# Kernel optimization log

Measured on AMD Instinct MI355X. Metric: run time of the kernel, lower is better.

Reference implementation:

```python
import jax, jax.numpy as jnp
import numpy as np

TEMPERATURE = 0.07
EPS = 1e-12  # F.normalize clamp


def _project(x, We, be, W1, b1, W2, b2):
    # encoder Linear then projection head Linear->ReLU->Linear
    h = x @ We + be                      # [B, 512]
    h = jax.nn.relu(h @ W1 + b1)         # [B, 256]
    return h @ W2 + b2                   # [B, 128]


def _ntxent(z1, z2, t):
    B = z1.shape[0]
    z1 = z1 / jnp.maximum(jnp.linalg.norm(z1, axis=1, keepdims=True), EPS)
    z2 = z2 / jnp.maximum(jnp.linalg.norm(z2, axis=1, keepdims=True), EPS)
    reps = jnp.concatenate([z1, z2], axis=0)          # [2B, 128]
    sim = reps @ reps.T                               # [2B, 2B]
    N = 2 * B
    idx = jnp.arange(N)
    # positives: eye rolled by B along columns -> column (i+B) mod N
    pos = sim[idx, (idx + B) % N][:, None]            # [N, 1]
    # negatives: all off-diagonal entries per row, in column order
    cols = jnp.arange(N - 1)[None, :]                 # [1, N-1]
    neg_idx = cols + (cols >= idx[:, None])           # skip the diagonal
    neg = jnp.take_along_axis(sim, neg_idx, axis=1)   # [N, N-1]
    logits = jnp.concatenate([pos, neg], axis=1) / t  # [N, N]
    # cross-entropy with label 0
    return jnp.mean(jax.nn.logsumexp(logits, axis=1) - logits[:, 0])


def setup_inputs() -> dict:
    key = jax.random.key(0)
    ks = jax.random.split(key, 10)
    B, Din, Denc, Dh, Dp = 4096, 1024, 512, 256, 128
    s = lambda fan_in: 1.0 / np.sqrt(fan_in)
    return {
        "x_image": jax.random.normal(ks[0], (B, Din), jnp.float32),
        "x_text": jax.random.normal(ks[1], (B, Din), jnp.float32),
        "We_img": jax.random.normal(ks[2], (Din, Denc), jnp.float32) * s(Din),
        "be_img": jnp.zeros((Denc,), jnp.float32),
        "We_txt": jax.random.normal(ks[3], (Din, Denc), jnp.float32) * s(Din),
        "be_txt": jnp.zeros((Denc,), jnp.float32),
        "Wp1_img": jax.random.normal(ks[4], (Denc, Dh), jnp.float32) * s(Denc),
        "bp1_img": jnp.zeros((Dh,), jnp.float32),
        "Wp2_img": jax.random.normal(ks[5], (Dh, Dp), jnp.float32) * s(Dh),
        "bp2_img": jnp.zeros((Dp,), jnp.float32),
        "Wp1_txt": jax.random.normal(ks[6], (Denc, Dh), jnp.float32) * s(Denc),
        "bp1_txt": jnp.zeros((Dh,), jnp.float32),
        "Wp2_txt": jax.random.normal(ks[7], (Dh, Dp), jnp.float32) * s(Dh),
        "bp2_txt": jnp.zeros((Dp,), jnp.float32),
    }


def reference(x_image, x_text, We_img, be_img, We_txt, be_txt,
              Wp1_img, bp1_img, Wp2_img, bp2_img,
              Wp1_txt, bp1_txt, Wp2_txt, bp2_txt):
    z1 = _project(x_image, We_img, be_img, Wp1_img, bp1_img, Wp2_img, bp2_img)
    z2 = _project(x_text, We_txt, be_txt, Wp1_txt, bp1_txt, Wp2_txt, bp2_txt)
    # single modality pair ('image','text') -> one NT-Xent loss
    return _ntxent(z1, z2, TEMPERATURE)
```

## Files before the change

### kernel.cpp

```cpp
#include <hip/hip_runtime.h>
#include <hip/hip_bf16.h>
#include <math.h>

typedef __bf16 bf16_t;
typedef __bf16 bf8 __attribute__((ext_vector_type(8)));
typedef __bf16 bf4 __attribute__((ext_vector_type(4)));
typedef __bf16 bf16x2 __attribute__((ext_vector_type(2)));
typedef float f32x4 __attribute__((ext_vector_type(4)));

#define AS1 __attribute__((address_space(1)))
#define AS3 __attribute__((address_space(3)))

#define B_ROWS 4096
#define NTOT   8192
#define DIN    1024
#define DENC   512
#define DH     256
#define DP     128
#define NSLICE 16
#define INV_T        14.285714285714286f
#define SCALE_LOG2   20.609929155556620f

__device__ __forceinline__ f32x4 mfma_16x16x32(bf8 a, bf8 b, f32x4 c) {
  return __builtin_amdgcn_mfma_f32_16x16x32_bf16(a, b, c, 0, 0, 0);
}

__global__ __launch_bounds__(256) void prep_kernel(
    const float* __restrict__ x_i, const float* __restrict__ x_t,
    const float* __restrict__ We_i, const float* __restrict__ We_t,
    const float* __restrict__ W1_i, const float* __restrict__ W1_t,
    const float* __restrict__ W2_i, const float* __restrict__ W2_t,
    bf16_t* __restrict__ xb_i, bf16_t* __restrict__ xb_t,
    bf16_t* __restrict__ Wet_i, bf16_t* __restrict__ Wet_t,
    bf16_t* __restrict__ W1t_i, bf16_t* __restrict__ W1t_t,
    bf16_t* __restrict__ W2t_i, bf16_t* __restrict__ W2t_t) {
  const int b = blockIdx.x;
  const int tid = threadIdx.x;
  if (b >= 336) {
    int idx = (b - 336) * 256 + tid;
    const int HALF = (B_ROWS * DIN) / 4;
    const float* s; bf16_t* d; int off;
    if (idx < HALF) { s = x_i; d = xb_i; off = idx; }
    else            { s = x_t; d = xb_t; off = idx - HALF; }
    float4 v = ((const float4*)s)[off];
    bf4 w = { (bf16_t)v.x, (bf16_t)v.y, (bf16_t)v.z, (bf16_t)v.w };
    ((bf4*)d)[off] = w;
    return;
  }
  const float* src; bf16_t* dst; int K, N, tile;
  if (b < 128)      { src = We_i; dst = Wet_i; K = 1024; N = 512; tile = b; }
  else if (b < 256) { src = We_t; dst = Wet_t; K = 1024; N = 512; tile = b - 128; }
  else if (b < 288) { src = W1_i; dst = W1t_i; K = 512;  N = 256; tile = b - 256; }
  else if (b < 320) { src = W1_t; dst = W1t_t; K = 512;  N = 256; tile = b - 288; }
  else if (b < 328) { src = W2_i; dst = W2t_i; K = 256;  N = 128; tile = b - 320; }
  else              { src = W2_t; dst = W2t_t; K = 256;  N = 128; tile = b - 328; }
  const int tilesN = N >> 6;
  const int k0 = (tile / tilesN) * 64;
  const int n0 = (tile % tilesN) * 64;

  __shared__ float ld[64][65];
  #pragma unroll
  for (int i = 0; i < 4; ++i) {
    int cid = tid + i * 256;
    int r = cid >> 4;
    int c = (cid & 15) * 4;
    float4 v = *(const float4*)(src + (size_t)(k0 + r) * N + n0 + c);
    ld[r][c + 0] = v.x; ld[r][c + 1] = v.y; ld[r][c + 2] = v.z; ld[r][c + 3] = v.w;
  }
  __syncthreads();
  #pragma unroll
  for (int i = 0; i < 2; ++i) {
    int cid = tid + i * 256;
    int rn = cid >> 3;
    int c8 = (cid & 7) * 8;
    bf8 w;
    #pragma unroll
    for (int j = 0; j < 8; ++j) w[j] = (bf16_t)ld[c8 + j][rn];
    *(bf8*)(dst + (size_t)(n0 + rn) * K + k0 + c8) = w;
  }
}

template<int MT, bool RELU>
__global__ __launch_bounds__(256) void gemm_glds(
    const bf16_t* __restrict__ A0, const bf16_t* __restrict__ A1,
    const bf16_t* __restrict__ B0, const bf16_t* __restrict__ B1,
    const float* __restrict__ bias0, const float* __restrict__ bias1,
    bf16_t* __restrict__ out0, bf16_t* __restrict__ out1,
    int N, int K) {
  const bf16_t* A   = blockIdx.z ? A1 : A0;
  const bf16_t* Bt  = blockIdx.z ? B1 : B0;
  const float* bias = blockIdx.z ? bias1 : bias0;
  bf16_t* outp      = blockIdx.z ? out1 : out0;

  const int nb   = blockIdx.x * 64;
  const int mb   = blockIdx.y * MT;
  const int tid  = threadIdx.x;
  const int wave = tid >> 6;
  const int lane = tid & 63;
  const int l15  = lane & 15;
  const int quad = lane >> 4;
  constexpr int CH = MT / 64;

  __shared__ __align__(16) bf16_t As[2][MT * 32];
  __shared__ __align__(16) bf16_t Bs[2][64 * 32];

  f32x4 acc[CH][4];
  #pragma unroll
  for (int i = 0; i < CH; ++i)
    #pragma unroll
    for (int j = 0; j < 4; ++j) acc[i][j] = (f32x4){0.f, 0.f, 0.f, 0.f};

  auto stage = [&](int k0, int pb) {
    #pragma unroll
    for (int i = 0; i < CH; ++i) {
      const int s = tid + i * 256;
      const bf16_t* ga = A + (size_t)(mb + (s >> 2)) * K + k0 + (s & 3) * 8;
      __builtin_amdgcn_global_load_lds(
          (const AS1 void*)ga,
          (AS3 void*)(As[pb] + (size_t)(wave * 64 + i * 256) * 8), 16, 0, 0);
    }
    const bf16_t* gb = Bt + (size_t)(nb + (tid >> 2)) * K + k0 + (tid & 3) * 8;
    __builtin_amdgcn_global_load_lds(
        (const AS1 void*)gb,
        (AS3 void*)(Bs[pb] + (size_t)(wave * 64) * 8), 16, 0, 0);
  };

  stage(0, 0);
  const int T = K >> 5;
  for (int t = 0; t < T; ++t) {
    __syncthreads();
    if (t + 1 < T) stage((t + 1) << 5, (t + 1) & 1);
    const bf16_t* as = As[t & 1];
    const bf16_t* bs = Bs[t & 1];
    bf8 a[CH];
    #pragma unroll
    for (int i = 0; i < CH; ++i)
      a[i] = *(const bf8*)(as + (size_t)(wave * (16 * CH) + i * 16 + l15) * 32 + quad * 8);
    #pragma unroll
    for (int nt = 0; nt < 4; ++nt) {
      bf8 bb = *(const bf8*)(bs + (size_t)(nt * 16 + l15) * 32 + quad * 8);
      #pragma unroll
      for (int i = 0; i < CH; ++i)
        acc[i][nt] = mfma_16x16x32(a[i], bb, acc[i][nt]);
    }
  }

  #pragma unroll
  for (int i = 0; i < CH; ++i) {
    const int orow = mb + wave * (16 * CH) + i * 16 + quad * 4;
    #pragma unroll
    for (int nt = 0; nt < 4; ++nt) {
      const int ocol = nb + nt * 16 + l15;
      const float bval = bias[ocol];
      #pragma unroll
      for (int r = 0; r < 4; ++r) {
        float v = acc[i][nt][r] + bval;
        if (RELU) v = fmaxf(v, 0.f);
        outp[(size_t)(orow + r) * N + ocol] = (bf16_t)v;
      }
    }
  }
}

__global__ __launch_bounds__(256) void head2_norm(
    const bf16_t* __restrict__ A0, const bf16_t* __restrict__ A1,
    const bf16_t* __restrict__ B0, const bf16_t* __restrict__ B1,
    const float* __restrict__ bias0, const float* __restrict__ bias1,
    bf16_t* __restrict__ reps) {
  const bf16_t* A   = blockIdx.z ? A1 : A0;
  const bf16_t* Bt  = blockIdx.z ? B1 : B0;
  const float* bias = blockIdx.z ? bias1 : bias0;

  const int mb   = blockIdx.x * 16;
  const int tid  = threadIdx.x;
  const int wave = tid >> 6;
  const int lane = tid & 63;
  const int l15  = lane & 15;
  const int quad = lane >> 4;
  const int wc0  = wave * 32;

  __shared__ __align__(16) bf16_t Asb[2][16 * 32];
  __shared__ __align__(16) bf16_t Bsb[2][128 * 32];
  __shared__ float ssL[64];

  f32x4 acc[2];
  acc[0] = (f32x4){0.f, 0.f, 0.f, 0.f};
  acc[1] = (f32x4){0.f, 0.f, 0.f, 0.f};

  auto stage = [&](int k0, int pb) {
    if (wave == 0) {
      const int row = lane >> 2, j = lane & 3, cf = j ^ (row & 3);
      const bf16_t* ga = A + (size_t)(mb + row) * DH + k0 + cf * 8;
      __builtin_amdgcn_global_load_lds(
          (const AS1 void*)ga, (AS3 void*)(Asb[pb]), 16, 0, 0);
    }
    #pragma unroll
    for (int i = 0; i < 2; ++i) {
      const int s = wave * 64 + i * 256 + lane;
      const int col = s >> 2, j = s & 3, cf = j ^ (col & 3);
      const bf16_t* gb = Bt + (size_t)col * DH + k0 + cf * 8;
      __builtin_amdgcn_global_load_lds(
          (const AS1 void*)gb,
          (AS3 void*)(Bsb[pb] + (size_t)(wave * 64 + i * 256) * 8), 16, 0, 0);
    }
  };

  stage(0, 0);
  for (int t = 0; t < 8; ++t) {
    __syncthreads();
    if (t < 7) stage((t + 1) << 5, (t + 1) & 1);
    const bf16_t* as = Asb[t & 1];
    const bf16_t* bs = Bsb[t & 1];
    bf8 a = *(const bf8*)(as + (size_t)(l15 * 4 + (quad ^ (l15 & 3))) * 8);
    #pragma unroll
    for (int nt = 0; nt < 2; ++nt) {
      const int col = wc0 + nt * 16 + l15;
      bf8 bb = *(const bf8*)(bs + (size_t)(col * 4 + (quad ^ (col & 3))) * 8);
      acc[nt] = mfma_16x16x32(a, bb, acc[nt]);
    }
  }

  float ssp[4];
  #pragma unroll
  for (int r = 0; r < 4; ++r) {
    #pragma unroll
    for (int nt = 0; nt < 2; ++nt) acc[nt][r] += bias[wc0 + nt * 16 + l15];
    float s = acc[0][r] * acc[0][r] + acc[1][r] * acc[1][r];
    s += __shfl_xor(s, 1); s += __shfl_xor(s, 2);
    s += __shfl_xor(s, 4); s += __shfl_xor(s, 8);
    ssp[r] = s;
  }
  if (l15 == 0) {
    #pragma unroll
    for (int r = 0; r < 4; ++r) ssL[wave * 16 + quad * 4 + r] = ssp[r];
  }
  __syncthreads();
  const size_t gr0 = (size_t)(blockIdx.z ? B_ROWS : 0) + mb + quad * 4;
  #pragma unroll
  for (int r = 0; r < 4; ++r) {
    const int row = quad * 4 + r;
    float tot = ssL[row] + ssL[16 + row] + ssL[32 + row] + ssL[48 + row];
    const float inv = 1.0f / fmaxf(sqrtf(tot), 1e-12f);
    #pragma unroll
    for (int nt = 0; nt < 2; ++nt)
      reps[(gr0 + r) * DP + wc0 + nt * 16 + l15] = (bf16_t)(acc[nt][r] * inv);
  }
}

__global__ __launch_bounds__(256) void sim_rowsum_kernel(
    const bf16_t* __restrict__ reps, float* __restrict__ Spart) {
  const int rowbase = blockIdx.y * 256;
  const int slice   = blockIdx.x;
  const int col0    = slice * 512;
  const int tid  = threadIdx.x;
  const int wave = tid >> 6;
  const int lane = tid & 63;
  const int l15  = lane & 15;
  const int quad = lane >> 4;

  __shared__ __align__(16) bf16_t Bs[2][64 * DP];

  const int r0 = rowbase + wave * 64;
  bf8 af[4][4];
  #pragma unroll
  for (int c = 0; c < 4; ++c)
    #pragma unroll
    for (int kt = 0; kt < 4; ++kt)
      af[c][kt] = *(const bf8*)(reps + (size_t)(r0 + c * 16 + l15) * DP + kt * 32 + quad * 8);

  float rs[4][4];
  #pragma unroll
  for (int c = 0; c < 4; ++c)
    #pragma unroll
    for (int r = 0; r < 4; ++r) rs[c][r] = 0.f;

  for (int t = 0; t < 8; ++t) {
    bf16_t* buf = Bs[t & 1];
    __syncthreads();
    const int jt0 = col0 + t * 64;
    #pragma unroll
    for (int r = 0; r < 4; ++r) {
      const int s   = r * 256 + tid;
      const int col = s >> 4;
      const int cf  = (s & 15) ^ (col & 15);
      const bf16_t* g = reps + (size_t)(jt0 + col) * DP + cf * 8;
      __builtin_amdgcn_global_load_lds(
          (const AS1 void*)g,
          (AS3 void*)(buf + (size_t)(r * 256 + wave * 64) * 8), 16, 0, 0);
    }
    __syncthreads();

    #pragma unroll
    for (int st = 0; st < 4; ++st) {
      const bf16_t* base = buf + (size_t)(st * 16 + l15) * DP;
      bf8 b0 = *(const bf8*)(base + (((0 * 4 + quad) ^ l15) * 8));
      bf8 b1 = *(const bf8*)(base + (((1 * 4 + quad) ^ l15) * 8));
      bf8 b2 = *(const bf8*)(base + (((2 * 4 + quad) ^ l15) * 8));
      bf8 b3 = *(const bf8*)(base + (((3 * 4 + quad) ^ l15) * 8));
      #pragma unroll
      for (int c = 0; c < 4; ++c) {
        f32x4 acc = (f32x4){0.f, 0.f, 0.f, 0.f};
        acc = mfma_16x16x32(af[c][0], b0, acc);
        acc = mfma_16x16x32(af[c][1], b1, acc);
        acc = mfma_16x16x32(af[c][2], b2, acc);
        acc = mfma_16x16x32(af[c][3], b3, acc);
        #pragma unroll
        for (int r = 0; r < 4; ++r)
          rs[c][r] += __builtin_amdgcn_exp2f(acc[r] * SCALE_LOG2);
      }
    }
  }

  #pragma unroll
  for (int c = 0; c < 4; ++c) {
    const int i0 = r0 + c * 16 + quad * 4;
    #pragma unroll
    for (int r = 0; r < 4; ++r) {
      float v = rs[c][r];
      v += __shfl_xor(v, 1); v += __shfl_xor(v, 2);
      v += __shfl_xor(v, 4); v += __shfl_xor(v, 8);
      if (l15 == 0) Spart[(size_t)slice * NTOT + i0 + r] = v;
    }
  }
}

__global__ __launch_bounds__(256) void rowfinal_kernel(
    const bf16_t* __restrict__ reps, const float* __restrict__ Spart,
    float* __restrict__ L) {
  const int tid  = threadIdx.x;
  const int wave = tid >> 6;
  const int lane = tid & 63;
  const int row  = blockIdx.x * 4 + wave;
  bf16x2 a = *(const bf16x2*)(reps + (size_t)row * DP + lane * 2);
  bf16x2 b = *(const bf16x2*)(reps + (size_t)(row ^ B_ROWS) * DP + lane * 2);
  float a0 = (float)a.x, a1 = (float)a.y;
  float b0 = (float)b.x, b1 = (float)b.y;
  float dii = a0 * a0 + a1 * a1;
  float pos = a0 * b0 + a1 * b1;
  float ps  = (lane < NSLICE) ? Spart[(size_t)lane * NTOT + row] : 0.f;
  #pragma unroll
  for (int m = 1; m < 64; m <<= 1) {
    dii += __shfl_xor(dii, m);
    pos += __shfl_xor(pos, m);
    ps  += __shfl_xor(ps, m);
  }
  if (lane == 0) {
    float Si = ps - __builtin_amdgcn_exp2f(dii * SCALE_LOG2)
                  + __builtin_amdgcn_exp2f(pos * SCALE_LOG2);
    L[row] = logf(Si) - pos * INV_T;
  }
}

__global__ __launch_bounds__(1024) void reduce_kernel(
    const float* __restrict__ L, float* __restrict__ out) {
  const int tid = threadIdx.x;
  float acc = 0.f;
  for (int i = tid; i < NTOT; i += 1024) acc += L[i];
  #pragma unroll
  for (int m = 1; m < 64; m <<= 1) acc += __shfl_xor(acc, m);
  __shared__ float wsum[16];
  if ((tid & 63) == 0) wsum[tid >> 6] = acc;
  __syncthreads();
  if (tid < 16) {
    float v = wsum[tid];
    #pragma unroll
    for (int m = 1; m < 16; m <<= 1) v += __shfl_xor(v, m);
    if (tid == 0) out[0] = v * (1.0f / NTOT);
  }
}

extern "C" void kernel_launch(void* const* d_in, const int* in_sizes, int n_in,
                              void* d_out, int out_size, void* d_ws, size_t ws_size,
                              hipStream_t stream) {
  const float* x_img  = (const float*)d_in[0];
  const float* x_txt  = (const float*)d_in[1];
  const float* We_img = (const float*)d_in[2];
  const float* be_img = (const float*)d_in[3];
  const float* We_txt = (const float*)d_in[4];
  const float* be_txt = (const float*)d_in[5];
  const float* W1_img = (const float*)d_in[6];
  const float* b1_img = (const float*)d_in[7];
  const float* W2_img = (const float*)d_in[8];
  const float* b2_img = (const float*)d_in[9];
  const float* W1_txt = (const float*)d_in[10];
  const float* b1_txt = (const float*)d_in[11];
  const float* W2_txt = (const float*)d_in[12];
  const float* b2_txt = (const float*)d_in[13];

  char* p = (char*)d_ws;
  bf16_t* xbf_img = (bf16_t*)p; p += (size_t)B_ROWS * DIN * 2;
  bf16_t* xbf_txt = (bf16_t*)p; p += (size_t)B_ROWS * DIN * 2;
  bf16_t* Wet_img = (bf16_t*)p; p += (size_t)DENC * DIN * 2;
  bf16_t* Wet_txt = (bf16_t*)p; p += (size_t)DENC * DIN * 2;
  bf16_t* W1t_img = (bf16_t*)p; p += (size_t)DH * DENC * 2;
  bf16_t* W1t_txt = (bf16_t*)p; p += (size_t)DH * DENC * 2;
  bf16_t* W2t_img = (bf16_t*)p; p += (size_t)DP * DH * 2;
  bf16_t* W2t_txt = (bf16_t*)p; p += (size_t)DP * DH * 2;
  bf16_t* h_img   = (bf16_t*)p; p += (size_t)B_ROWS * DENC * 2;
  bf16_t* h_txt   = (bf16_t*)p; p += (size_t)B_ROWS * DENC * 2;
  bf16_t* g_img   = (bf16_t*)p; p += (size_t)B_ROWS * DH * 2;
  bf16_t* g_txt   = (bf16_t*)p; p += (size_t)B_ROWS * DH * 2;
  bf16_t* reps    = (bf16_t*)p; p += (size_t)NTOT * DP * 2;
  float*  Spart   = (float*) p; p += (size_t)NSLICE * NTOT * 4;
  float*  L       = (float*) p; p += (size_t)NTOT * 4;

  prep_kernel<<<336 + 8192, 256, 0, stream>>>(
      x_img, x_txt, We_img, We_txt, W1_img, W1_txt, W2_img, W2_txt,
      xbf_img, xbf_txt, Wet_img, Wet_txt, W1t_img, W1t_txt, W2t_img, W2t_txt);

  gemm_glds<128, false><<<dim3(DENC / 64, B_ROWS / 128, 2), 256, 0, stream>>>(
      xbf_img, xbf_txt, Wet_img, Wet_txt, be_img, be_txt, h_img, h_txt,
      DENC, DIN);
  gemm_glds<64, true><<<dim3(DH / 64, B_ROWS / 64, 2), 256, 0, stream>>>(
      h_img, h_txt, W1t_img, W1t_txt, b1_img, b1_txt, g_img, g_txt,
      DH, DENC);
  head2_norm<<<dim3(B_ROWS / 16, 1, 2), 256, 0, stream>>>(
      g_img, g_txt, W2t_img, W2t_txt, b2_img, b2_txt, reps);

  sim_rowsum_kernel<<<dim3(NSLICE, NTOT / 256), 256, 0, stream>>>(reps, Spart);
  rowfinal_kernel<<<NTOT / 4, 256, 0, stream>>>(reps, Spart, L);
  reduce_kernel<<<1, 1024, 0, stream>>>(L, (float*)d_out);
}
```

Baseline: 181.3 us.

## Quantize normalized reps to FP8 and use scaled FP8 MFMA for similarity

Adds a kernel that converts the normalized bf16 representations to FP8 (e4m3). The similarity/exp row-sum kernel then uses the 16x16x128 f8f6f4 scaled MFMA, with each lane loading 32 bytes of fp8 per row instead of four bf8 fragments. The column slice count is doubled so each block covers 256 columns. The goal is to cut MFMA issue count and LDS/global traffic in the dominant 8192x8192 similarity pass, at the cost of one extra launch and reduced precision in logits scaled by 1/0.07. The diagonal and positive terms in rowfinal are recomputed from the fp8 data so they stay consistent with the fp8 sums.

```diff
diff --git a/kernel.cpp b/kernel.cpp
--- a/kernel.cpp
+++ b/kernel.cpp
@@ -7,6 +7,8 @@
 typedef __bf16 bf4 __attribute__((ext_vector_type(4)));
 typedef __bf16 bf16x2 __attribute__((ext_vector_type(2)));
 typedef float f32x4 __attribute__((ext_vector_type(4)));
+typedef int i32x8 __attribute__((ext_vector_type(8)));
+typedef unsigned char u8;
 
 #define AS1 __attribute__((address_space(1)))
 #define AS3 __attribute__((address_space(3)))
@@ -17,7 +19,7 @@
 #define DENC   512
 #define DH     256
 #define DP     128
-#define NSLICE 16
+#define NSLICE 32
 #define INV_T        14.285714285714286f
 #define SCALE_LOG2   20.609929155556620f
 
@@ -247,63 +249,81 @@
   }
 }
 
-__global__ __launch_bounds__(256) void sim_rowsum_kernel(
-    const bf16_t* __restrict__ reps, float* __restrict__ Spart) {
+__global__ __launch_bounds__(256) void quant_kernel(
+    const bf16_t* __restrict__ reps, u8* __restrict__ reps8) {
+  const int idx = blockIdx.x * 256 + threadIdx.x;
+  bf8 v = ((const bf8*)reps)[idx];
+  float f[8];
+  #pragma unroll
+  for (int j = 0; j < 8; ++j) f[j] = (float)v[j];
+  int u0 = __builtin_amdgcn_cvt_pk_fp8_f32(f[0], f[1], 0, 0);
+  u0 = __builtin_amdgcn_cvt_pk_fp8_f32(f[2], f[3], u0, 1);
+  int u1 = __builtin_amdgcn_cvt_pk_fp8_f32(f[4], f[5], 0, 0);
+  u1 = __builtin_amdgcn_cvt_pk_fp8_f32(f[6], f[7], u1, 1);
+  uint2 o; o.x = (unsigned)u0; o.y = (unsigned)u1;
+  ((uint2*)reps8)[idx] = o;
+}
+
+__global__ __launch_bounds__(256) void sim_fp8_kernel(
+    const u8* __restrict__ reps8, float* __restrict__ Spart) {
   const int rowbase = blockIdx.y * 256;
   const int slice   = blockIdx.x;
-  const int col0    = slice * 512;
+  const int col0    = slice * 256;
   const int tid  = threadIdx.x;
   const int wave = tid >> 6;
   const int lane = tid & 63;
   const int l15  = lane & 15;
   const int quad = lane >> 4;
 
-  __shared__ __align__(16) bf16_t Bs[2][64 * DP];
+  __shared__ __align__(16) u8 Bs[2][64 * DP];
 
   const int r0 = rowbase + wave * 64;
-  bf8 af[4][4];
+  i32x8 af[4];
+  #pragma unroll
+  for (int c = 0; c < 4; ++c) {
+    const uint4* ap = (const uint4*)(reps8 + (size_t)(r0 + c * 16 + l15) * DP + quad * 32);
+    uint4 x0 = ap[0], x1 = ap[1];
+    af[c] = (i32x8){(int)x0.x, (int)x0.y, (int)x0.z, (int)x0.w,
+                    (int)x1.x, (int)x1.y, (int)x1.z, (int)x1.w};
+  }
+
+  float rs[4][4];
   #pragma unroll
   for (int c = 0; c < 4; ++c)
     #pragma unroll
-    for (int kt = 0; kt < 4; ++kt)
-      af[c][kt] = *(const bf8*)(reps + (size_t)(r0 + c * 16 + l15) * DP + kt * 32 + quad * 8);
-
-  float rs[4][4];
-  #pragma unroll
-  for (int c = 0; c < 4; ++c)
-    #pragma unroll
     for (int r = 0; r < 4; ++r) rs[c][r] = 0.f;
 
-  for (int t = 0; t < 8; ++t) {
-    bf16_t* buf = Bs[t & 1];
+  for (int t = 0; t < 4; ++t) {
+    u8* buf = Bs[t & 1];
     __syncthreads();
     const int jt0 = col0 + t * 64;
     #pragma unroll
-    for (int r = 0; r < 4; ++r) {
-      const int s   = r * 256 + tid;
-      const int col = s >> 4;
-      const int cf  = (s & 15) ^ (col & 15);
-      const bf16_t* g = reps + (size_t)(jt0 + col) * DP + cf * 8;
+    for (int i = 0; i < 2; ++i) {
+      const int s   = i * 256 + tid;
+      const int col = s >> 3;
+      const int cf  = (s & 7) ^ (col & 7);
+      const u8* g = reps8 + (size_t)(jt0 + col) * DP + cf * 16;
       __builtin_amdgcn_global_load_lds(
           (const AS1 void*)g,
-          (AS3 void*)(buf + (size_t)(r * 256 + wave * 64) * 8), 16, 0, 0);
+          (AS3 void*)(buf + (size_t)(i * 256 + wave * 64) * 16), 16, 0, 0);
     }
     __syncthreads();
 
     #pragma unroll
     for (int st = 0; st < 4; ++st) {
-      const bf16_t* base = buf + (size_t)(st * 16 + l15) * DP;
-      bf8 b0 = *(const bf8*)(base + (((0 * 4 + quad) ^ l15) * 8));
-      bf8 b1 = *(const bf8*)(base + (((1 * 4 + quad) ^ l15) * 8));
-      bf8 b2 = *(const bf8*)(base + (((2 * 4 + quad) ^ l15) * 8));
-      bf8 b3 = *(const bf8*)(base + (((3 * 4 + quad) ^ l15) * 8));
+      const int coln = st * 16 + l15;
+      const u8* cbase = buf + (size_t)coln * DP;
+      const int c0 = ((2 * quad)     ^ (coln & 7)) * 16;
+      const int c1 = ((2 * quad + 1) ^ (coln & 7)) * 16;
+      uint4 b0 = *(const uint4*)(cbase + c0);
+      uint4 b1 = *(const uint4*)(cbase + c1);
+      i32x8 bf = (i32x8){(int)b0.x, (int)b0.y, (int)b0.z, (int)b0.w,
+                         (int)b1.x, (int)b1.y, (int)b1.z, (int)b1.w};
       #pragma unroll
       for (int c = 0; c < 4; ++c) {
         f32x4 acc = (f32x4){0.f, 0.f, 0.f, 0.f};
-        acc = mfma_16x16x32(af[c][0], b0, acc);
-        acc = mfma_16x16x32(af[c][1], b1, acc);
-        acc = mfma_16x16x32(af[c][2], b2, acc);
-        acc = mfma_16x16x32(af[c][3], b3, acc);
+        acc = __builtin_amdgcn_mfma_scale_f32_16x16x128_f8f6f4(
+            af[c], bf, acc, 0, 0, 0, 0x7F7F7F7F, 0, 0x7F7F7F7F);
         #pragma unroll
         for (int r = 0; r < 4; ++r)
           rs[c][r] += __builtin_amdgcn_exp2f(acc[r] * SCALE_LOG2);
@@ -325,16 +345,18 @@
 }
 
 __global__ __launch_bounds__(256) void rowfinal_kernel(
-    const bf16_t* __restrict__ reps, const float* __restrict__ Spart,
+    const u8* __restrict__ reps8, const float* __restrict__ Spart,
     float* __restrict__ L) {
   const int tid  = threadIdx.x;
   const int wave = tid >> 6;
   const int lane = tid & 63;
   const int row  = blockIdx.x * 4 + wave;
-  bf16x2 a = *(const bf16x2*)(reps + (size_t)row * DP + lane * 2);
-  bf16x2 b = *(const bf16x2*)(reps + (size_t)(row ^ B_ROWS) * DP + lane * 2);
-  float a0 = (float)a.x, a1 = (float)a.y;
-  float b0 = (float)b.x, b1 = (float)b.y;
+  const int ua = *(const unsigned short*)(reps8 + (size_t)row * DP + lane * 2);
+  const int ub = *(const unsigned short*)(reps8 + (size_t)(row ^ B_ROWS) * DP + lane * 2);
+  float a0 = __builtin_amdgcn_cvt_f32_fp8(ua, 0);
+  float a1 = __builtin_amdgcn_cvt_f32_fp8(ua, 1);
+  float b0 = __builtin_amdgcn_cvt_f32_fp8(ub, 0);
+  float b1 = __builtin_amdgcn_cvt_f32_fp8(ub, 1);
   float dii = a0 * a0 + a1 * a1;
   float pos = a0 * b0 + a1 * b1;
   float ps  = (lane < NSLICE) ? Spart[(size_t)lane * NTOT + row] : 0.f;
@@ -401,6 +423,7 @@
   bf16_t* g_img   = (bf16_t*)p; p += (size_t)B_ROWS * DH * 2;
   bf16_t* g_txt   = (bf16_t*)p; p += (size_t)B_ROWS * DH * 2;
   bf16_t* reps    = (bf16_t*)p; p += (size_t)NTOT * DP * 2;
+  u8*     reps8   = (u8*)    p; p += (size_t)NTOT * DP;
   float*  Spart   = (float*) p; p += (size_t)NSLICE * NTOT * 4;
   float*  L       = (float*) p; p += (size_t)NTOT * 4;
 
@@ -417,7 +440,8 @@
   head2_norm<<<dim3(B_ROWS / 16, 1, 2), 256, 0, stream>>>(
       g_img, g_txt, W2t_img, W2t_txt, b2_img, b2_txt, reps);
 
-  sim_rowsum_kernel<<<dim3(NSLICE, NTOT / 256), 256, 0, stream>>>(reps, Spart);
-  rowfinal_kernel<<<NTOT / 4, 256, 0, stream>>>(reps, Spart, L);
+  quant_kernel<<<(NTOT * DP / 8) / 256, 256, 0, stream>>>(reps, reps8);
+  sim_fp8_kernel<<<dim3(NSLICE, NTOT / 256), 256, 0, stream>>>(reps8, Spart);
+  rowfinal_kernel<<<NTOT / 4, 256, 0, stream>>>(reps8, Spart, L);
   reduce_kernel<<<1, 1024, 0, stream>>>(L, (float*)d_out);
 }
```

New measurement: 178.8 us. No clear change (-1.4%).
